# Optimization experiments

Hardware: AMD Instinct MI355X
Metric: run time of the kernel (lower is better)

The kernel has to match this reference:

```python
import jax, jax.numpy as jnp
import numpy as np

GROUP = 4      # number of groups in the batch dim
SHARED_GP = 4  # conv groups for q/k 1x1 convs
C = 512
N = 4096
B = 4          # B_all = GROUP * B = 16
EPS_LN = 1e-6
EPS_Z = 1e-6


def _phi(x):
    return jax.nn.relu(x) + 1.0


def _grouped_1x1(x, W):
    # x: [B, C, N], W: [g, C/g, C/g] block-diagonal 1x1 conv weights
    Bx, Cx, Nx = x.shape
    g = W.shape[0]
    xg = x.reshape(Bx, g, Cx // g, Nx)
    return jnp.einsum('goc,bgcn->bgon', W, xg).reshape(Bx, Cx, Nx)


def _ln(x, w, b, eps=EPS_LN):
    m = jnp.mean(x, axis=-1, keepdims=True)
    v = jnp.mean(jnp.square(x - m), axis=-1, keepdims=True)
    return (x - m) * jax.lax.rsqrt(v + eps) * w + b


def setup_inputs() -> dict:
    key = jax.random.key(0)
    ks = jax.random.split(key, 12)
    cg = C // SHARED_GP
    s = 1.0 / np.sqrt(C)
    return {
        'x': jax.random.normal(ks[0], (GROUP * B, C, N), dtype=jnp.float32),
        'Wq': jax.random.normal(ks[1], (SHARED_GP, cg, cg), dtype=jnp.float32) / np.sqrt(cg),
        'Wk': jax.random.normal(ks[2], (SHARED_GP, cg, cg), dtype=jnp.float32) / np.sqrt(cg),
        'Wv': jax.random.normal(ks[3], (C, C), dtype=jnp.float32) * s,
        'Wphi': jax.random.normal(ks[4], (C, C), dtype=jnp.float32) * s,
        'ln1_w': jnp.ones((C,), dtype=jnp.float32),
        'ln1_b': jnp.zeros((C,), dtype=jnp.float32),
        'fc1_w': jax.random.normal(ks[5], (4 * C, C), dtype=jnp.float32) * s,
        'fc1_b': jnp.zeros((4 * C,), dtype=jnp.float32),
        'fc2_w': jax.random.normal(ks[6], (C, 4 * C), dtype=jnp.float32) / np.sqrt(4 * C),
        'fc2_b': jnp.zeros((C,), dtype=jnp.float32),
        'ln2_w': jnp.ones((C,), dtype=jnp.float32),
        'ln2_b': jnp.zeros((C,), dtype=jnp.float32),
    }


def reference(x, Wq, Wk, Wv, Wphi, ln1_w, ln1_b, fc1_w, fc1_b, fc2_w, fc2_b, ln2_w, ln2_b):
    B_all, Cc, Nn = x.shape
    g = GROUP
    Bb = B_all // g
    first, rest = x[:Bb], x[Bb:]             # [B,C,N], [M,C,N] with M=(g-1)*B
    M = (g - 1) * Bb

    q = _phi(_grouped_1x1(rest, Wq))          # [M,C,N]
    k0 = _phi(_grouped_1x1(first, Wk))        # [B,C,N]
    v0 = jnp.einsum('oc,bcn->bon', Wv, first)  # [B,C,N]
    phi_first = jnp.einsum('oc,bcn->bon', Wphi, first)
    phi_rest = jnp.einsum('oc,bcn->bon', Wphi, rest)

    # expand first-group k/v across the (g-1) query groups
    k = jnp.broadcast_to(k0[None], (g - 1, Bb, Cc, Nn)).reshape(M, Cc, Nn)
    v = jnp.broadcast_to(v0[None], (g - 1, Bb, Cc, Nn)).reshape(M, Cc, Nn)

    Qg = jnp.broadcast_to(k0.mean(axis=2, keepdims=True)[None],
                          (g - 1, Bb, Cc, 1)).reshape(M, Cc, 1)
    alpha = jax.nn.softmax(jnp.sum(Qg * k, axis=1, keepdims=True), axis=-1) * Nn  # [M,1,N]
    k_hat = k * alpha

    # linear attention: kv = k_hat @ v^T / sqrt(C)
    kv = jnp.einsum('mcn,mdn->mcd', k_hat, v) / jnp.sqrt(jnp.asarray(Cc, x.dtype))  # [M,C,C]
    k_sum = jnp.sum(k_hat, axis=-1)                                  # [M,C]
    z = 1.0 / (jnp.einsum('mcn,mc->mn', q, k_sum)[:, None, :] + EPS_Z)  # [M,1,N]
    y = jnp.einsum('mcn,mcd->mdn', q, kv) * z * phi_rest              # [M,C,N]

    y_first = jnp.mean(y, axis=0, keepdims=True) * phi_first          # [B,C,N]
    out_first = _ln((first + y_first).transpose(0, 2, 1), ln1_w, ln1_b)  # [B,N,C]
    h = jax.nn.relu(out_first @ fc1_w.T + fc1_b)
    out_first = out_first + h @ fc2_w.T + fc2_b
    out_first = jax.nn.relu(_ln(out_first, ln2_w, ln2_b))
    out_first = out_first.transpose(0, 2, 1)                          # [B,C,N]
    return jnp.concatenate([out_first, rest], axis=0)
```

## Files before the change

kernel.cpp:

```cpp
#include <hip/hip_runtime.h>

#define N_DIM 4096
#define C_DIM 512
#define CN_ ((long)C_DIM * (long)N_DIM)

typedef unsigned short ushort_t;
typedef __attribute__((ext_vector_type(8))) short bf16x8;
typedef __attribute__((ext_vector_type(4))) float f32x4;

typedef const __attribute__((address_space(1))) unsigned int* gas_t;
typedef __attribute__((address_space(3))) unsigned int* las_t;
#define GLOAD(g, l) __builtin_amdgcn_global_load_lds((gas_t)(g), (las_t)(l), 16, 0, 0)

__device__ __forceinline__ ushort_t f2b(float f) {
    unsigned u = __builtin_bit_cast(unsigned, f);
    u += 0x7fffu + ((u >> 16) & 1u);
    return (ushort_t)(u >> 16);
}
__device__ __forceinline__ float b2f(ushort_t s) {
    return __builtin_bit_cast(float, (unsigned)s << 16);
}

enum { EPI_NONE = 0, EPI_PHI = 1, EPI_RELU_BIAS = 2, EPI_RES_BIAS = 3, EPI_PRE = 4 };

#define STAGE(q, koff) { \
    GLOAD(ap0 + (koff), &Als[q][la0]); \
    GLOAD(ap1 + (koff), &Als[q][la1]); \
    GLOAD(bp0 + (koff), &Bls[q][la0]); \
    GLOAD(bp1 + (koff), &Bls[q][la1]); }

#define COMPUTE(q) { \
    bf16x8 af[4], bfv[4]; \
    _Pragma("unroll") for (int m_ = 0; m_ < 4; ++m_) \
        af[m_] = *(const bf16x8*)&Als[q][(wr + m_ * 16 + fr) * 32 + rsw]; \
    _Pragma("unroll") for (int nf_ = 0; nf_ < 4; ++nf_) \
        bfv[nf_] = *(const bf16x8*)&Bls[q][(wc + nf_ * 16 + fr) * 32 + rsw]; \
    _Pragma("unroll") for (int m_ = 0; m_ < 4; ++m_) \
        _Pragma("unroll") for (int nf_ = 0; nf_ < 4; ++nf_) \
            acc[m_][nf_] = __builtin_amdgcn_mfma_f32_16x16x32_bf16( \
                af[m_], bfv[nf_], acc[m_][nf_], 0, 0, 0); }

#define KLOOP(K_) { \
    STAGE(0, 0); \
    __syncthreads(); \
    int kk_ = 0; \
    while (true) { \
        if (kk_ + 32 < (K_)) STAGE(1, kk_ + 32); \
        COMPUTE(0); \
        __syncthreads(); \
        kk_ += 32; \
        if (kk_ >= (K_)) break; \
        if (kk_ + 32 < (K_)) STAGE(0, kk_ + 32); \
        COMPUTE(1); \
        __syncthreads(); \
        kk_ += 32; \
        if (kk_ >= (K_)) break; \
    } }

template<int EPI, bool GROUPED, bool OBF, bool DEN>
__global__ __launch_bounds__(256, 3) void mfma_gemm(
    const ushort_t* __restrict__ Wb, const ushort_t* __restrict__ A,
    void* __restrict__ OUTV, const float* __restrict__ bias,
    const ushort_t* __restrict__ auxb, const float* __restrict__ auxf,
    int K, int O, int a_rstride, long a_zstride, long o_zstride, long auxb_zstride,
    int xt, int yt)
{
    __shared__ ushort_t Als[2][128 * 32];
    __shared__ ushort_t Bls[2][128 * 32];
    const int tid = threadIdx.x;

    const int L = blockIdx.x;
    const int gpx = (gridDim.x >> 3) / xt;
    const int xcd = L & 7;
    const int j = L >> 3;
    const int xtile = j % xt;
    const int g = xcd * gpx + j / xt;
    const int ytile = g % yt;
    const int z = g / yt;

    const int o0 = xtile * 128;
    const int n0 = ytile * 128;
    const ushort_t* Az = A + (long)z * a_zstride;
    const ushort_t* Wp = Wb;
    int kbase = 0, obase = o0;
    if (GROUPED) { int gg = o0 >> 7; Wp = Wb + (long)gg * (128 * 128); kbase = gg << 7; obase = 0; }

    const int w = tid >> 6, l = tid & 63;
    const int lr = l >> 2, lg = l & 3;
    const int rA0 = w * 32 + lr, rA1 = w * 32 + 16 + lr;
    const int gA0 = lg ^ ((rA0 >> 1) & 3), gA1 = lg ^ ((rA1 >> 1) & 3);
    const ushort_t* ap0 = Az + (long)(n0 + rA0) * a_rstride + kbase + gA0 * 8;
    const ushort_t* ap1 = Az + (long)(n0 + rA1) * a_rstride + kbase + gA1 * 8;
    const ushort_t* bp0 = Wp + (long)(obase + rA0) * K + gA0 * 8;
    const ushort_t* bp1 = Wp + (long)(obase + rA1) * K + gA1 * 8;
    const int la0 = (w * 32) * 32, la1 = (w * 32 + 16) * 32;

    const int wr = (w >> 1) * 64, wc = (w & 1) * 64;
    const int fr = l & 15, ks = l >> 4;
    const int rsw = (ks ^ ((fr >> 1) & 3)) << 3;

    f32x4 acc[4][4];
#pragma unroll
    for (int m = 0; m < 4; ++m)
#pragma unroll
        for (int nf = 0; nf < 4; ++nf) acc[m][nf] = f32x4{0.f, 0.f, 0.f, 0.f};

    KLOOP(K);

    float dsum[4][4];
    if (DEN) {
#pragma unroll
        for (int m = 0; m < 4; ++m)
#pragma unroll
            for (int j2 = 0; j2 < 4; ++j2) dsum[m][j2] = 0.f;
    }

#pragma unroll
    for (int m = 0; m < 4; ++m) {
#pragma unroll
        for (int nf = 0; nf < 4; ++nf) {
            const int oo = o0 + wc + nf * 16 + fr;
            float bval = 0.f;
            if (EPI == EPI_RELU_BIAS || EPI == EPI_RES_BIAS) bval = bias[oo];
            float kw = 0.f;
            if (DEN) kw = bias[((z & 3) << 9) + oo];
#pragma unroll
            for (int j2 = 0; j2 < 4; ++j2) {
                const int nn = n0 + wr + m * 16 + ks * 4 + j2;
                const long ridx = (long)nn * O + oo;
                float v = acc[m][nf][j2];
                if (EPI == EPI_PHI)            v = fmaxf(v, 0.f) + 1.f;
                else if (EPI == EPI_RELU_BIAS) v = fmaxf(v + bval, 0.f);
                else if (EPI == EPI_RES_BIAS)  v = v + bval + b2f(auxb[(long)z * auxb_zstride + ridx]);
                else if (EPI == EPI_PRE)       v = b2f(auxb[(long)z * auxb_zstride + ridx]) + auxf[ridx] * v;
                if (DEN) dsum[m][j2] += v * kw;
                if (OBF) ((ushort_t*)OUTV)[(long)z * o_zstride + ridx] = f2b(v);
                else     ((float*)OUTV)[(long)z * o_zstride + ridx] = v;
            }
        }
    }

    if (DEN) {
#pragma unroll
        for (int m = 0; m < 4; ++m)
#pragma unroll
            for (int j2 = 0; j2 < 4; ++j2) {
                float d = dsum[m][j2];
                d += __shfl_xor(d, 1); d += __shfl_xor(d, 2);
                d += __shfl_xor(d, 4); d += __shfl_xor(d, 8);
                if (fr == 0) {
                    const int nn = n0 + wr + m * 16 + ks * 4 + j2;
                    atomicAdd((float*)&auxf[(long)z * N_DIM + nn], d);
                }
            }
    }
}

__global__ __launch_bounds__(256, 3) void kv_mfma(
    const ushort_t* __restrict__ v0c, const ushort_t* __restrict__ khat,
    float* __restrict__ kvb)
{
    __shared__ ushort_t Als[2][128 * 32];
    __shared__ ushort_t Bls[2][128 * 32];
    const int tid = threadIdx.x;
    const int L = blockIdx.x;
    const int gpx = (gridDim.x >> 3) >> 2;
    const int xcd = L & 7;
    const int j = L >> 3;
    const int xtile = j & 3;
    const int g = xcd * gpx + (j >> 2);
    const int ytile = g & 3;
    const int z = g >> 2;
    const int c0 = xtile * 128, d0 = ytile * 128;
    const int b = z >> 3, nch = z & 7;

    const int w = tid >> 6, l = tid & 63;
    const int lr = l >> 2, lg = l & 3;
    const int rA0 = w * 32 + lr, rA1 = w * 32 + 16 + lr;
    const int gA0 = lg ^ ((rA0 >> 1) & 3), gA1 = lg ^ ((rA1 >> 1) & 3);
    const ushort_t* Ab = v0c + (long)b * CN_ + nch * 512;
    const ushort_t* Bb = khat + (long)b * CN_ + nch * 512;
    const ushort_t* ap0 = Ab + (long)(d0 + rA0) * N_DIM + gA0 * 8;
    const ushort_t* ap1 = Ab + (long)(d0 + rA1) * N_DIM + gA1 * 8;
    const ushort_t* bp0 = Bb + (long)(c0 + rA0) * N_DIM + gA0 * 8;
    const ushort_t* bp1 = Bb + (long)(c0 + rA1) * N_DIM + gA1 * 8;
    const int la0 = (w * 32) * 32, la1 = (w * 32 + 16) * 32;

    const int wr = (w >> 1) * 64, wc = (w & 1) * 64;
    const int fr = l & 15, ks = l >> 4;
    const int rsw = (ks ^ ((fr >> 1) & 3)) << 3;

    f32x4 acc[4][4];
#pragma unroll
    for (int m = 0; m < 4; ++m)
#pragma unroll
        for (int nf = 0; nf < 4; ++nf) acc[m][nf] = f32x4{0.f, 0.f, 0.f, 0.f};

    KLOOP(512);

    float* KV = kvb + (long)b * 262144;
#pragma unroll
    for (int m = 0; m < 4; ++m)
#pragma unroll
        for (int nf = 0; nf < 4; ++nf) {
            const int cc = c0 + wc + nf * 16 + fr;
#pragma unroll
            for (int j2 = 0; j2 < 4; ++j2) {
                const int dd = d0 + wr + m * 16 + ks * 4 + j2;
                atomicAdd(&KV[(long)dd * 512 + cc], acc[m][nf][j2]);
            }
        }
}

__global__ __launch_bounds__(256, 2) void ybar_gemm(
    const ushort_t* __restrict__ q12, const ushort_t* __restrict__ kvT,
    const ushort_t* __restrict__ xT12, const ushort_t* __restrict__ Wphi_b,
    const float* __restrict__ den12, ushort_t* __restrict__ y12)
{
    __shared__ ushort_t Als[2][128 * 32];
    __shared__ ushort_t Bls[2][128 * 32];
    const int tid = threadIdx.x;
    const int L = blockIdx.x;
    const int gpx = (gridDim.x >> 3) >> 2;
    const int xcd = L & 7;
    const int j = L >> 3;
    const int xtile = j & 3;
    const int g = xcd * gpx + (j >> 2);
    const int ytile = g & 31;
    const int mm = g >> 5;
    const int o0 = xtile * 128, n0 = ytile * 128;

    const int w = tid >> 6, l = tid & 63;
    const int lr = l >> 2, lg = l & 3;
    const int rA0 = w * 32 + lr, rA1 = w * 32 + 16 + lr;
    const int gA0 = lg ^ ((rA0 >> 1) & 3), gA1 = lg ^ ((rA1 >> 1) & 3);
    const long aoff0 = (long)(n0 + rA0) * 512 + gA0 * 8;
    const long aoff1 = (long)(n0 + rA1) * 512 + gA1 * 8;
    const long boff0 = (long)(o0 + rA0) * 512 + gA0 * 8;
    const long boff1 = (long)(o0 + rA1) * 512 + gA1 * 8;
    const int la0 = (w * 32) * 32, la1 = (w * 32 + 16) * 32;

    const int wr = (w >> 1) * 64, wc = (w & 1) * 64;
    const int fr = l & 15, ks = l >> 4;
    const int rsw = (ks ^ ((fr >> 1) & 3)) << 3;

    f32x4 acc[4][4];
#pragma unroll
    for (int m = 0; m < 4; ++m)
#pragma unroll
        for (int nf = 0; nf < 4; ++nf) acc[m][nf] = f32x4{0.f, 0.f, 0.f, 0.f};

    const ushort_t* ap0 = xT12 + (long)mm * CN_ + aoff0;
    const ushort_t* ap1 = xT12 + (long)mm * CN_ + aoff1;
    const ushort_t* bp0 = Wphi_b + boff0;
    const ushort_t* bp1 = Wphi_b + boff1;
    KLOOP(512);

    uint2 ph[4][4];
#pragma unroll
    for (int m = 0; m < 4; ++m)
#pragma unroll
        for (int nf = 0; nf < 4; ++nf) {
            ph[m][nf].x = (unsigned)f2b(acc[m][nf][0]) | ((unsigned)f2b(acc[m][nf][1]) << 16);
            ph[m][nf].y = (unsigned)f2b(acc[m][nf][2]) | ((unsigned)f2b(acc[m][nf][3]) << 16);
            acc[m][nf] = f32x4{0.f, 0.f, 0.f, 0.f};
        }

    ap0 = q12 + (long)mm * CN_ + aoff0;
    ap1 = q12 + (long)mm * CN_ + aoff1;
    bp0 = kvT + (long)(mm & 3) * 262144 + boff0;
    bp1 = kvT + (long)(mm & 3) * 262144 + boff1;
    KLOOP(512);

    const float* D = den12 + (long)mm * N_DIM;
    ushort_t* Y = y12 + (long)mm * CN_;
#pragma unroll
    for (int m = 0; m < 4; ++m) {
        float zr[4];
#pragma unroll
        for (int j2 = 0; j2 < 4; ++j2)
            zr[j2] = 1.f / (D[n0 + wr + m * 16 + ks * 4 + j2] + 1e-6f);
#pragma unroll
        for (int nf = 0; nf < 4; ++nf) {
            const int oo = o0 + wc + nf * 16 + fr;
            float pv[4];
            pv[0] = b2f((ushort_t)(ph[m][nf].x & 0xffff));
            pv[1] = b2f((ushort_t)(ph[m][nf].x >> 16));
            pv[2] = b2f((ushort_t)(ph[m][nf].y & 0xffff));
            pv[3] = b2f((ushort_t)(ph[m][nf].y >> 16));
#pragma unroll
            for (int j2 = 0; j2 < 4; ++j2) {
                const int nn = n0 + wr + m * 16 + ks * 4 + j2;
                Y[(long)nn * 512 + oo] = f2b(acc[m][nf][j2] * zr[j2] * pv[j2]);
            }
        }
    }
}

__global__ __launch_bounds__(256) void ybar_reduce(
    const ushort_t* __restrict__ y12, float* __restrict__ ybar)
{
    const long i = ((long)blockIdx.x * 256 + threadIdx.x) * 8;
    float s[8] = {0.f, 0.f, 0.f, 0.f, 0.f, 0.f, 0.f, 0.f};
    for (int mm = 0; mm < 12; ++mm) {
        uint4 u = *(const uint4*)&y12[(long)mm * CN_ + i];
        const ushort_t* us = (const ushort_t*)&u;
#pragma unroll
        for (int j = 0; j < 8; ++j) s[j] += b2f(us[j]);
    }
#pragma unroll
    for (int j = 0; j < 8; ++j) s[j] *= (1.f / 12.f);
    *(float4*)&ybar[i] = make_float4(s[0], s[1], s[2], s[3]);
    *(float4*)&ybar[i + 4] = make_float4(s[4], s[5], s[6], s[7]);
}

__global__ __launch_bounds__(256) void cvt_scale(
    const float* __restrict__ in, ushort_t* __restrict__ out)
{
    const float s = 0.044194173824159216f;
    int i = (blockIdx.x * 256 + threadIdx.x) * 4;
    float4 v = *(const float4*)&in[i];
    union { ushort_t sh[4]; uint2 u; } p;
    p.sh[0] = f2b(v.x * s); p.sh[1] = f2b(v.y * s);
    p.sh[2] = f2b(v.z * s); p.sh[3] = f2b(v.w * s);
    *(uint2*)&out[i] = p.u;
}

template<int ALPHA>
__global__ __launch_bounds__(256) void transpose_b2b(
    const ushort_t* __restrict__ in, ushort_t* __restrict__ out,
    const float* __restrict__ alpha)
{
    __shared__ ushort_t t[64][72];
    const int tid = threadIdx.x;
    const int n0 = blockIdx.x * 64, c0 = blockIdx.y * 64, z = blockIdx.z;
    const ushort_t* I = in + (long)z * CN_;
    ushort_t* O = out + (long)z * CN_;
    const int r = tid >> 2, s8 = (tid & 3) * 16;
    uint4 u0 = *(const uint4*)&I[(long)(n0 + r) * 512 + c0 + s8];
    uint4 u1 = *(const uint4*)&I[(long)(n0 + r) * 512 + c0 + s8 + 8];
    *(uint4*)&t[r][s8] = u0;
    *(uint4*)&t[r][s8 + 8] = u1;
    __syncthreads();
    union { ushort_t sh[16]; uint4 u[2]; } p;
#pragma unroll
    for (int i = 0; i < 16; ++i) {
        ushort_t v = t[s8 + i][r];
        if (ALPHA) v = f2b(b2f(v) * alpha[(long)z * N_DIM + n0 + s8 + i]);
        p.sh[i] = v;
    }
    uint4* dst = (uint4*)&O[(long)(c0 + r) * N_DIM + n0 + s8];
    dst[0] = p.u[0]; dst[1] = p.u[1];
}

__global__ __launch_bounds__(256) void cvt_all(
    const float* __restrict__ s0, ushort_t* __restrict__ d0,
    const float* __restrict__ s1, ushort_t* __restrict__ d1,
    const float* __restrict__ s2, ushort_t* __restrict__ d2,
    const float* __restrict__ s3, ushort_t* __restrict__ d3,
    const float* __restrict__ s4, ushort_t* __restrict__ d4,
    const float* __restrict__ s5, ushort_t* __restrict__ d5)
{
    long i = ((long)blockIdx.x * 256 + threadIdx.x) * 4;
    const float* s; ushort_t* d; long off;
    if (i < 65536)        { s = s0; d = d0; off = i; }
    else if (i < 131072)  { s = s1; d = d1; off = i - 65536; }
    else if (i < 393216)  { s = s2; d = d2; off = i - 131072; }
    else if (i < 655360)  { s = s3; d = d3; off = i - 393216; }
    else if (i < 1703936) { s = s4; d = d4; off = i - 655360; }
    else                  { s = s5; d = d5; off = i - 1703936; }
    float4 v = *(const float4*)&s[off];
    union { ushort_t sh[4]; uint2 u; } p;
    p.sh[0] = f2b(v.x); p.sh[1] = f2b(v.y); p.sh[2] = f2b(v.z); p.sh[3] = f2b(v.w);
    *(uint2*)&d[off] = p.u;
}

template<int PASSZ>
__global__ __launch_bounds__(256) void transpose_f2b(
    const float* __restrict__ in, ushort_t* __restrict__ out,
    int rows, int cols, long in_z, long out_z, float* __restrict__ passout)
{
    __shared__ float t[64][65];
    const int tid = threadIdx.x;
    const int n0 = blockIdx.x * 64, c0 = blockIdx.y * 64;
    const int z = blockIdx.z;
    const float* I = in + (long)z * in_z;
    ushort_t* Ot = out + (long)z * out_z;
    const int r = tid >> 2, s4 = (tid & 3) * 16;
    float4 raw[4];
#pragma unroll
    for (int i = 0; i < 16; i += 4) {
        float4 v = *(const float4*)&I[(long)(c0 + r) * cols + n0 + s4 + i];
        raw[i >> 2] = v;
        t[r][s4 + i] = v.x; t[r][s4 + i + 1] = v.y;
        t[r][s4 + i + 2] = v.z; t[r][s4 + i + 3] = v.w;
    }
    if (PASSZ && z >= 4) {
        float* P = passout + (long)z * in_z + (long)(c0 + r) * cols + n0 + s4;
#pragma unroll
        for (int i = 0; i < 4; ++i) *(float4*)&P[i * 4] = raw[i];
    }
    __syncthreads();
    union { ushort_t s[16]; uint4 u[2]; } pk;
#pragma unroll
    for (int i = 0; i < 16; ++i) pk.s[i] = f2b(t[s4 + i][r]);
    uint4* dst = (uint4*)&Ot[(long)(n0 + r) * rows + c0 + s4];
    dst[0] = pk.u[0]; dst[1] = pk.u[1];
}

__global__ __launch_bounds__(256) void colreduce_part(
    const ushort_t* __restrict__ X, const float* __restrict__ wgt,
    float* __restrict__ part)
{
    const int ns = blockIdx.x, b = blockIdx.y;
    const int tid = threadIdx.x;
    const int w = tid >> 6, l = tid & 63;
    const int c8 = l * 8;
    const ushort_t* Xb = X + (long)b * CN_;
    float acc[8] = {0.f, 0.f, 0.f, 0.f, 0.f, 0.f, 0.f, 0.f};
    for (int r = w; r < 128; r += 4) {
        const int n = ns * 128 + r;
        uint4 u = *(const uint4*)&Xb[(long)n * C_DIM + c8];
        const ushort_t* us = (const ushort_t*)&u;
        const float wv = wgt ? wgt[(long)b * N_DIM + n] : 1.f;
#pragma unroll
        for (int i = 0; i < 8; ++i) acc[i] += b2f(us[i]) * wv;
    }
    __shared__ float red[4][512];
#pragma unroll
    for (int i = 0; i < 8; ++i) red[w][c8 + i] = acc[i];
    __syncthreads();
    for (int c = tid; c < 512; c += 256) {
        part[((long)ns * 4 + b) * C_DIM + c] =
            red[0][c] + red[1][c] + red[2][c] + red[3][c];
    }
}

__global__ __launch_bounds__(256) void colreduce_fin(
    const float* __restrict__ part, float* __restrict__ out, float scale)
{
    int b = blockIdx.x;
    for (int c = threadIdx.x; c < 512; c += 256) {
        float s = 0.f;
        for (int ns = 0; ns < 32; ++ns) s += part[((long)ns * 4 + b) * C_DIM + c];
        out[b * C_DIM + c] = s * scale;
    }
}

__global__ __launch_bounds__(256) void dot_rows(
    const ushort_t* __restrict__ X, const float* __restrict__ w,
    float* __restrict__ out)
{
    const int tid = threadIdx.x;
    const int rn = tid >> 2, cs = (tid & 3) * 128;
    const int z = blockIdx.y;
    const int n = blockIdx.x * 64 + rn;
    const ushort_t* row = X + (long)z * CN_ + (long)n * C_DIM;
    const float* wz = w + (long)(z & 3) * C_DIM;
    float s = 0.f;
    for (int i = 0; i < 128; i += 8) {
        uint4 u = *(const uint4*)&row[cs + i];
        const ushort_t* us = (const ushort_t*)&u;
#pragma unroll
        for (int k2 = 0; k2 < 8; ++k2) s += b2f(us[k2]) * wz[cs + i + k2];
    }
    s += __shfl_xor(s, 1); s += __shfl_xor(s, 2);
    if ((tid & 3) == 0) out[(long)z * N_DIM + n] = s;
}

__global__ __launch_bounds__(256) void softmax_alpha(
    const float* __restrict__ logits, float* __restrict__ alpha)
{
    int b = blockIdx.x, tid = threadIdx.x;
    const float* L = logits + (long)b * N_DIM;
    float* A = alpha + (long)b * N_DIM;
    float lv[16];
    float mx = -3.4e38f;
#pragma unroll
    for (int i = 0; i < 4; i++) {
        float4 v = *(const float4*)&L[tid * 4 + i * 1024];
        lv[4 * i + 0] = v.x; lv[4 * i + 1] = v.y; lv[4 * i + 2] = v.z; lv[4 * i + 3] = v.w;
        mx = fmaxf(mx, fmaxf(fmaxf(v.x, v.y), fmaxf(v.z, v.w)));
    }
    __shared__ float red[8];
    float m = mx;
#pragma unroll
    for (int off = 32; off; off >>= 1) m = fmaxf(m, __shfl_down(m, off, 64));
    int wid = tid >> 6, lane = tid & 63;
    if (lane == 0) red[wid] = m;
    __syncthreads();
    m = fmaxf(fmaxf(red[0], red[1]), fmaxf(red[2], red[3]));
    float e[16], s = 0.f;
#pragma unroll
    for (int i = 0; i < 16; i++) { e[i] = expf(lv[i] - m); s += e[i]; }
#pragma unroll
    for (int off = 32; off; off >>= 1) s += __shfl_down(s, off, 64);
    if (lane == 0) red[4 + wid] = s;
    __syncthreads();
    float S = red[4] + red[5] + red[6] + red[7];
    float sc = 4096.f / S;
#pragma unroll
    for (int i = 0; i < 4; i++)
        *(float4*)&A[tid * 4 + i * 1024] =
            make_float4(e[4 * i] * sc, e[4 * i + 1] * sc, e[4 * i + 2] * sc, e[4 * i + 3] * sc);
}

template<int RELU, int OBF, int IBF>
__global__ __launch_bounds__(256) void ln_row(
    const void* __restrict__ inv, const float* __restrict__ g,
    const float* __restrict__ bt, void* __restrict__ outv)
{
    const int tid = threadIdx.x;
    const int r = tid >> 3, cs = (tid & 7) * 64;
    const long base = (((long)blockIdx.y * N_DIM) + blockIdx.x * 32 + r) * C_DIM + cs;
    float vv[64];
    float s = 0.f, s2 = 0.f;
    if (IBF) {
        const ushort_t* I = (const ushort_t*)inv + base;
#pragma unroll
        for (int i = 0; i < 8; ++i) {
            uint4 u = *(const uint4*)&I[i * 8];
            const ushort_t* us = (const ushort_t*)&u;
#pragma unroll
            for (int jj = 0; jj < 8; ++jj) {
                float f = b2f(us[jj]); vv[i * 8 + jj] = f; s += f; s2 += f * f;
            }
        }
    } else {
        const float* I = (const float*)inv + base;
#pragma unroll
        for (int i = 0; i < 16; ++i) {
            float4 v = *(const float4*)&I[i * 4];
            vv[i * 4] = v.x; vv[i * 4 + 1] = v.y; vv[i * 4 + 2] = v.z; vv[i * 4 + 3] = v.w;
            s += v.x + v.y + v.z + v.w;
            s2 += v.x * v.x + v.y * v.y + v.z * v.z + v.w * v.w;
        }
    }
#pragma unroll
    for (int off = 1; off < 8; off <<= 1) { s += __shfl_xor(s, off); s2 += __shfl_xor(s2, off); }
    const float mean = s * (1.f / 512.f);
    const float var = s2 * (1.f / 512.f) - mean * mean;
    const float rs = rsqrtf(var + 1e-6f);
#pragma unroll
    for (int i = 0; i < 64; i += 4) {
        float o[4];
#pragma unroll
        for (int jj = 0; jj < 4; ++jj) {
            float ov = (vv[i + jj] - mean) * rs * g[cs + i + jj] + bt[cs + i + jj];
            if (RELU) ov = fmaxf(ov, 0.f);
            o[jj] = ov;
        }
        if (OBF) {
            union { ushort_t s4[4]; uint2 u; } p;
            p.s4[0] = f2b(o[0]); p.s4[1] = f2b(o[1]); p.s4[2] = f2b(o[2]); p.s4[3] = f2b(o[3]);
            *(uint2*)&((ushort_t*)outv)[base + i] = p.u;
        } else {
            *(float4*)&((float*)outv)[base + i] = make_float4(o[0], o[1], o[2], o[3]);
        }
    }
}

__global__ __launch_bounds__(256) void ln_tr(
    const ushort_t* __restrict__ in, const float* __restrict__ g,
    const float* __restrict__ bt, float* __restrict__ out)
{
    __shared__ float t[32][513];
    const int tid = threadIdx.x;
    const int r = tid >> 3;
    const int lc = (tid & 7) * 8;
    const int z = blockIdx.y;
    const long n = (long)blockIdx.x * 32 + r;
    const ushort_t* I = in + ((long)z * N_DIM + n) * C_DIM;
    float vv[64];
    float s = 0.f, s2 = 0.f;
#pragma unroll
    for (int i = 0; i < 8; ++i) {
        const int c = i * 64 + lc;
        uint4 u = *(const uint4*)&I[c];
        const ushort_t* us = (const ushort_t*)&u;
#pragma unroll
        for (int jj = 0; jj < 8; ++jj) {
            float f = b2f(us[jj]); vv[i * 8 + jj] = f; s += f; s2 += f * f;
        }
    }
#pragma unroll
    for (int off = 1; off < 8; off <<= 1) { s += __shfl_xor(s, off); s2 += __shfl_xor(s2, off); }
    const float mean = s * (1.f / 512.f);
    const float var = s2 * (1.f / 512.f) - mean * mean;
    const float rs = rsqrtf(var + 1e-6f);
#pragma unroll
    for (int i = 0; i < 8; ++i) {
        const int c = i * 64 + lc;
#pragma unroll
        for (int jj = 0; jj < 8; ++jj) {
            float o = (vv[i * 8 + jj] - mean) * rs * g[c + jj] + bt[c + jj];
            t[r][c + jj] = fmaxf(o, 0.f);
        }
    }
    __syncthreads();
    float* O = out + (long)z * CN_ + (long)blockIdx.x * 32;
    for (int c = tid; c < 512; c += 256) {
        float* dst = O + (long)c * N_DIM;
#pragma unroll
        for (int i = 0; i < 32; i += 4)
            *(float4*)&dst[i] = make_float4(t[i][c], t[i + 1][c], t[i + 2][c], t[i + 3][c]);
    }
}

extern "C" void kernel_launch(void* const* d_in, const int* in_sizes, int n_in,
                              void* d_out, int out_size, void* d_ws, size_t ws_size,
                              hipStream_t stream)
{
    const float* x     = (const float*)d_in[0];
    const float* Wq    = (const float*)d_in[1];
    const float* Wk    = (const float*)d_in[2];
    const float* Wv    = (const float*)d_in[3];
    const float* Wphi  = (const float*)d_in[4];
    const float* ln1_w = (const float*)d_in[5];
    const float* ln1_b = (const float*)d_in[6];
    const float* fc1_w = (const float*)d_in[7];
    const float* fc1_bias = (const float*)d_in[8];
    const float* fc2_w = (const float*)d_in[9];
    const float* fc2_bias = (const float*)d_in[10];
    const float* ln2_w = (const float*)d_in[11];
    const float* ln2_b = (const float*)d_in[12];
    float* out = (float*)d_out;

    float* ws = (float*)d_ws;
    const long CN = CN_;
    ushort_t* xTfirst = (ushort_t*)ws;
    ushort_t* tln     = (ushort_t*)ws;
    ushort_t* xT12 = (ushort_t*)(ws + 2 * CN);
    ushort_t* hbuf4 = (ushort_t*)(ws + 2 * CN);
    ushort_t* q12   = (ushort_t*)(ws + 8 * CN);
    ushort_t* y12   = (ushort_t*)(ws + 14 * CN);
    ushort_t* k0b = (ushort_t*)(ws + 20 * CN);
    ushort_t* v0b = (ushort_t*)(ws + 22 * CN);
    ushort_t* pre_b = (ushort_t*)(ws + 20 * CN);
    ushort_t* khat = (ushort_t*)(ws + 24 * CN);
    ushort_t* v0c  = (ushort_t*)(ws + 26 * CN);
    ushort_t* ubuf_b = (ushort_t*)(ws + 24 * CN);
    float* ybar = ws + 32 * CN;
    float* kvb  = ws + 33 * CN;
    ushort_t* kvT = (ushort_t*)(ws + 33 * CN + 1048576);
    float* wb = ws + 33 * CN + 1572864;
    ushort_t* Wk_b   = (ushort_t*)(wb);
    ushort_t* Wq_b   = (ushort_t*)(wb + 32768);
    ushort_t* Wv_b   = (ushort_t*)(wb + 65536);
    ushort_t* Wphi_b = (ushort_t*)(wb + 196608);
    ushort_t* fc1_b16 = (ushort_t*)(wb + 327680);
    ushort_t* fc2_b16 = (ushort_t*)(wb + 851968);
    float* part   = wb + 1376256;
    float* Qg     = wb + 1441792;
    float* ksum   = wb + 1443840;
    float* logits = wb + 1445888;
    float* alpha  = wb + 1462272;
    float* den12  = wb + 1478656;

    dim3 blk(256);

    cvt_all<<<2688, blk, 0, stream>>>(Wk, Wk_b, Wq, Wq_b, Wv, Wv_b,
                                      Wphi, Wphi_b, fc1_w, fc1_b16, fc2_w, fc2_b16);
    hipMemsetAsync(kvb, 0, 1048576 * sizeof(float), stream);
    hipMemsetAsync(den12, 0, 49152 * sizeof(float), stream);

    transpose_f2b<1><<<dim3(64, 8, 16), blk, 0, stream>>>(
        x, xTfirst, 512, 4096, CN, CN, out);

    mfma_gemm<EPI_PHI, true, true, false><<<512, blk, 0, stream>>>(
        Wk_b, xTfirst, k0b, nullptr, nullptr, nullptr, 128, 512, 512, CN, CN, 0, 4, 32);
    mfma_gemm<EPI_NONE, false, true, false><<<512, blk, 0, stream>>>(
        Wv_b, xTfirst, v0b, nullptr, nullptr, nullptr, 512, 512, 512, CN, CN, 0, 4, 32);
    colreduce_part<<<dim3(32, 4), blk, 0, stream>>>(k0b, nullptr, part);
    colreduce_fin<<<4, blk, 0, stream>>>(part, Qg, 1.f / 4096.f);
    dot_rows<<<dim3(64, 4), blk, 0, stream>>>(k0b, Qg, logits);
    softmax_alpha<<<4, blk, 0, stream>>>(logits, alpha);
    colreduce_part<<<dim3(32, 4), blk, 0, stream>>>(k0b, alpha, part);
    colreduce_fin<<<4, blk, 0, stream>>>(part, ksum, 1.f);
    transpose_b2b<1><<<dim3(64, 8, 4), blk, 0, stream>>>(k0b, khat, alpha);
    transpose_b2b<0><<<dim3(64, 8, 4), blk, 0, stream>>>(v0b, v0c, nullptr);
    kv_mfma<<<512, blk, 0, stream>>>(v0c, khat, kvb);
    cvt_scale<<<1024, blk, 0, stream>>>(kvb, kvT);

    mfma_gemm<EPI_PHI, true, true, true><<<1536, blk, 0, stream>>>(
        Wq_b, xT12, q12, ksum, nullptr, den12, 128, 512, 512, CN, CN, 0, 4, 32);
    ybar_gemm<<<1536, blk, 0, stream>>>(q12, kvT, xT12, Wphi_b, den12, y12);
    ybar_reduce<<<1024, blk, 0, stream>>>(y12, ybar);

    mfma_gemm<EPI_PRE, false, true, false><<<512, blk, 0, stream>>>(
        Wphi_b, xTfirst, pre_b, nullptr, xTfirst, ybar, 512, 512, 512, CN, CN, CN, 4, 32);
    ln_row<0, 1, 1><<<dim3(128, 4), blk, 0, stream>>>(pre_b, ln1_w, ln1_b, tln);
    mfma_gemm<EPI_RELU_BIAS, false, true, false><<<2048, blk, 0, stream>>>(
        fc1_b16, tln, hbuf4, fc1_bias, nullptr, nullptr,
        512, 2048, 512, CN, 8388608, 0, 16, 32);
    mfma_gemm<EPI_RES_BIAS, false, true, false><<<512, blk, 0, stream>>>(
        fc2_b16, hbuf4, ubuf_b, fc2_bias, tln, nullptr,
        2048, 512, 2048, 8388608, CN, CN, 4, 32);
    ln_tr<<<dim3(128, 4), blk, 0, stream>>>(ubuf_b, ln2_w, ln2_b, out);
}
```

Measured before the change: 497.0 us.

## Fuse column reductions into epilogues and replace kv atomics with partial buffers

```diff
diff --git a/kernel.cpp b/kernel.cpp
--- a/kernel.cpp
+++ b/kernel.cpp
@@ -57,7 +57,7 @@
         if (kk_ >= (K_)) break; \
     } }
 
-template<int EPI, bool GROUPED, bool OBF, bool DEN>
+template<int EPI, bool GROUPED, bool OBF, bool DEN, bool QGS>
 __global__ __launch_bounds__(256, 3) void mfma_gemm(
     const ushort_t* __restrict__ Wb, const ushort_t* __restrict__ A,
     void* __restrict__ OUTV, const float* __restrict__ bias,
@@ -114,6 +114,11 @@
 #pragma unroll
             for (int j2 = 0; j2 < 4; ++j2) dsum[m][j2] = 0.f;
     }
+    float qsum[4];
+    if (QGS) {
+#pragma unroll
+        for (int nf = 0; nf < 4; ++nf) qsum[nf] = 0.f;
+    }
 
 #pragma unroll
     for (int m = 0; m < 4; ++m) {
@@ -134,6 +139,7 @@
                 else if (EPI == EPI_RES_BIAS)  v = v + bval + b2f(auxb[(long)z * auxb_zstride + ridx]);
                 else if (EPI == EPI_PRE)       v = b2f(auxb[(long)z * auxb_zstride + ridx]) + auxf[ridx] * v;
                 if (DEN) dsum[m][j2] += v * kw;
+                if (QGS) qsum[nf] += v;
                 if (OBF) ((ushort_t*)OUTV)[(long)z * o_zstride + ridx] = f2b(v);
                 else     ((float*)OUTV)[(long)z * o_zstride + ridx] = v;
             }
@@ -154,11 +160,23 @@
                 }
             }
     }
+    if (QGS) {
+#pragma unroll
+        for (int nf = 0; nf < 4; ++nf) {
+            float d = qsum[nf];
+            d += __shfl_xor(d, 16);
+            d += __shfl_xor(d, 32);
+            if (ks == 0) {
+                const int oo = o0 + wc + nf * 16 + fr;
+                atomicAdd((float*)&auxf[((long)z << 9) + oo], d);
+            }
+        }
+    }
 }
 
 __global__ __launch_bounds__(256, 3) void kv_mfma(
     const ushort_t* __restrict__ v0c, const ushort_t* __restrict__ khat,
-    float* __restrict__ kvb)
+    float* __restrict__ kvp)
 {
     __shared__ ushort_t Als[2][128 * 32];
     __shared__ ushort_t Bls[2][128 * 32];
@@ -198,7 +216,7 @@
 
     KLOOP(512);
 
-    float* KV = kvb + (long)b * 262144;
+    float* KV = kvp + ((long)(nch * 4 + b)) * 262144;
 #pragma unroll
     for (int m = 0; m < 4; ++m)
 #pragma unroll
@@ -207,9 +225,28 @@
 #pragma unroll
             for (int j2 = 0; j2 < 4; ++j2) {
                 const int dd = d0 + wr + m * 16 + ks * 4 + j2;
-                atomicAdd(&KV[(long)dd * 512 + cc], acc[m][nf][j2]);
+                KV[(long)dd * 512 + cc] = acc[m][nf][j2];
             }
         }
+}
+
+__global__ __launch_bounds__(256) void cvt_scale8(
+    const float* __restrict__ kvp, ushort_t* __restrict__ out)
+{
+    const float s = 0.044194173824159216f;
+    const long i = ((long)blockIdx.x * 256 + threadIdx.x) * 4;
+    const int b = (int)(i >> 18);
+    const long j = i & 262143;
+    float4 a = make_float4(0.f, 0.f, 0.f, 0.f);
+#pragma unroll
+    for (int nch = 0; nch < 8; ++nch) {
+        float4 v = *(const float4*)&kvp[((long)(nch * 4 + b)) * 262144 + j];
+        a.x += v.x; a.y += v.y; a.z += v.z; a.w += v.w;
+    }
+    union { ushort_t sh[4]; uint2 u; } p;
+    p.sh[0] = f2b(a.x * s); p.sh[1] = f2b(a.y * s);
+    p.sh[2] = f2b(a.z * s); p.sh[3] = f2b(a.w * s);
+    *(uint2*)&out[i] = p.u;
 }
 
 __global__ __launch_bounds__(256, 2) void ybar_gemm(
@@ -314,22 +351,10 @@
     *(float4*)&ybar[i + 4] = make_float4(s[4], s[5], s[6], s[7]);
 }
 
-__global__ __launch_bounds__(256) void cvt_scale(
-    const float* __restrict__ in, ushort_t* __restrict__ out)
-{
-    const float s = 0.044194173824159216f;
-    int i = (blockIdx.x * 256 + threadIdx.x) * 4;
-    float4 v = *(const float4*)&in[i];
-    union { ushort_t sh[4]; uint2 u; } p;
-    p.sh[0] = f2b(v.x * s); p.sh[1] = f2b(v.y * s);
-    p.sh[2] = f2b(v.z * s); p.sh[3] = f2b(v.w * s);
-    *(uint2*)&out[i] = p.u;
-}
-
 template<int ALPHA>
 __global__ __launch_bounds__(256) void transpose_b2b(
     const ushort_t* __restrict__ in, ushort_t* __restrict__ out,
-    const float* __restrict__ alpha)
+    const float* __restrict__ alpha, float* __restrict__ ksum)
 {
     __shared__ ushort_t t[64][72];
     const int tid = threadIdx.x;
@@ -351,6 +376,16 @@
     }
     uint4* dst = (uint4*)&O[(long)(c0 + r) * N_DIM + n0 + s8];
     dst[0] = p.u[0]; dst[1] = p.u[1];
+    if (ALPHA) {
+        const int c = tid & 63, q = tid >> 6;
+        float s = 0.f;
+#pragma unroll
+        for (int i = 0; i < 16; ++i) {
+            const int n = q * 16 + i;
+            s += b2f(t[n][c]) * alpha[(long)z * N_DIM + n0 + n];
+        }
+        atomicAdd(&ksum[((long)z << 9) + c0 + c], s);
+    }
 }
 
 __global__ __launch_bounds__(256) void cvt_all(
@@ -408,48 +443,9 @@
     dst[0] = pk.u[0]; dst[1] = pk.u[1];
 }
 
-__global__ __launch_bounds__(256) void colreduce_part(
-    const ushort_t* __restrict__ X, const float* __restrict__ wgt,
-    float* __restrict__ part)
-{
-    const int ns = blockIdx.x, b = blockIdx.y;
-    const int tid = threadIdx.x;
-    const int w = tid >> 6, l = tid & 63;
-    const int c8 = l * 8;
-    const ushort_t* Xb = X + (long)b * CN_;
-    float acc[8] = {0.f, 0.f, 0.f, 0.f, 0.f, 0.f, 0.f, 0.f};
-    for (int r = w; r < 128; r += 4) {
-        const int n = ns * 128 + r;
-        uint4 u = *(const uint4*)&Xb[(long)n * C_DIM + c8];
-        const ushort_t* us = (const ushort_t*)&u;
-        const float wv = wgt ? wgt[(long)b * N_DIM + n] : 1.f;
-#pragma unroll
-        for (int i = 0; i < 8; ++i) acc[i] += b2f(us[i]) * wv;
-    }
-    __shared__ float red[4][512];
-#pragma unroll
-    for (int i = 0; i < 8; ++i) red[w][c8 + i] = acc[i];
-    __syncthreads();
-    for (int c = tid; c < 512; c += 256) {
-        part[((long)ns * 4 + b) * C_DIM + c] =
-            red[0][c] + red[1][c] + red[2][c] + red[3][c];
-    }
-}
-
-__global__ __launch_bounds__(256) void colreduce_fin(
-    const float* __restrict__ part, float* __restrict__ out, float scale)
-{
-    int b = blockIdx.x;
-    for (int c = threadIdx.x; c < 512; c += 256) {
-        float s = 0.f;
-        for (int ns = 0; ns < 32; ++ns) s += part[((long)ns * 4 + b) * C_DIM + c];
-        out[b * C_DIM + c] = s * scale;
-    }
-}
-
 __global__ __launch_bounds__(256) void dot_rows(
     const ushort_t* __restrict__ X, const float* __restrict__ w,
-    float* __restrict__ out)
+    float* __restrict__ out, float scale)
 {
     const int tid = threadIdx.x;
     const int rn = tid >> 2, cs = (tid & 3) * 128;
@@ -465,7 +461,7 @@
         for (int k2 = 0; k2 < 8; ++k2) s += b2f(us[k2]) * wz[cs + i + k2];
     }
     s += __shfl_xor(s, 1); s += __shfl_xor(s, 2);
-    if ((tid & 3) == 0) out[(long)z * N_DIM + n] = s;
+    if ((tid & 3) == 0) out[(long)z * N_DIM + n] = s * scale;
 }
 
 __global__ __launch_bounds__(256) void softmax_alpha(
@@ -641,59 +637,54 @@
     ushort_t* v0c  = (ushort_t*)(ws + 26 * CN);
     ushort_t* ubuf_b = (ushort_t*)(ws + 24 * CN);
     float* ybar = ws + 32 * CN;
-    float* kvb  = ws + 33 * CN;
-    ushort_t* kvT = (ushort_t*)(ws + 33 * CN + 1048576);
-    float* wb = ws + 33 * CN + 1572864;
+    float* kvp  = ws + 33 * CN;
+    ushort_t* kvT = (ushort_t*)(ws + 33 * CN + 8388608);
+    float* wb = ws + 33 * CN + 8388608 + 524288;
     ushort_t* Wk_b   = (ushort_t*)(wb);
     ushort_t* Wq_b   = (ushort_t*)(wb + 32768);
     ushort_t* Wv_b   = (ushort_t*)(wb + 65536);
     ushort_t* Wphi_b = (ushort_t*)(wb + 196608);
     ushort_t* fc1_b16 = (ushort_t*)(wb + 327680);
     ushort_t* fc2_b16 = (ushort_t*)(wb + 851968);
-    float* part   = wb + 1376256;
-    float* Qg     = wb + 1441792;
-    float* ksum   = wb + 1443840;
-    float* logits = wb + 1445888;
-    float* alpha  = wb + 1462272;
-    float* den12  = wb + 1478656;
+    float* Qg     = wb + 1376256;
+    float* ksum   = wb + 1378304;
+    float* logits = wb + 1380352;
+    float* alpha  = wb + 1396736;
+    float* den12  = wb + 1413120;
 
     dim3 blk(256);
 
     cvt_all<<<2688, blk, 0, stream>>>(Wk, Wk_b, Wq, Wq_b, Wv, Wv_b,
                                       Wphi, Wphi_b, fc1_w, fc1_b16, fc2_w, fc2_b16);
-    hipMemsetAsync(kvb, 0, 1048576 * sizeof(float), stream);
+    hipMemsetAsync(Qg, 0, 4096 * sizeof(float), stream);
     hipMemsetAsync(den12, 0, 49152 * sizeof(float), stream);
 
     transpose_f2b<1><<<dim3(64, 8, 16), blk, 0, stream>>>(
         x, xTfirst, 512, 4096, CN, CN, out);
 
-    mfma_gemm<EPI_PHI, true, true, false><<<512, blk, 0, stream>>>(
-        Wk_b, xTfirst, k0b, nullptr, nullptr, nullptr, 128, 512, 512, CN, CN, 0, 4, 32);
-    mfma_gemm<EPI_NONE, false, true, false><<<512, blk, 0, stream>>>(
+    mfma_gemm<EPI_PHI, true, true, false, true><<<512, blk, 0, stream>>>(
+        Wk_b, xTfirst, k0b, nullptr, nullptr, Qg, 128, 512, 512, CN, CN, 0, 4, 32);
+    mfma_gemm<EPI_NONE, false, true, false, false><<<512, blk, 0, stream>>>(
         Wv_b, xTfirst, v0b, nullptr, nullptr, nullptr, 512, 512, 512, CN, CN, 0, 4, 32);
-    colreduce_part<<<dim3(32, 4), blk, 0, stream>>>(k0b, nullptr, part);
-    colreduce_fin<<<4, blk, 0, stream>>>(part, Qg, 1.f / 4096.f);
-    dot_rows<<<dim3(64, 4), blk, 0, stream>>>(k0b, Qg, logits);
+    dot_rows<<<dim3(64, 4), blk, 0, stream>>>(k0b, Qg, logits, 1.f / 4096.f);
     softmax_alpha<<<4, blk, 0, stream>>>(logits, alpha);
-    colreduce_part<<<dim3(32, 4), blk, 0, stream>>>(k0b, alpha, part);
-    colreduce_fin<<<4, blk, 0, stream>>>(part, ksum, 1.f);
-    transpose_b2b<1><<<dim3(64, 8, 4), blk, 0, stream>>>(k0b, khat, alpha);
-    transpose_b2b<0><<<dim3(64, 8, 4), blk, 0, stream>>>(v0b, v0c, nullptr);
-    kv_mfma<<<512, blk, 0, stream>>>(v0c, khat, kvb);
-    cvt_scale<<<1024, blk, 0, stream>>>(kvb, kvT);
-
-    mfma_gemm<EPI_PHI, true, true, true><<<1536, blk, 0, stream>>>(
+    transpose_b2b<1><<<dim3(64, 8, 4), blk, 0, stream>>>(k0b, khat, alpha, ksum);
+    transpose_b2b<0><<<dim3(64, 8, 4), blk, 0, stream>>>(v0b, v0c, nullptr, nullptr);
+    kv_mfma<<<512, blk, 0, stream>>>(v0c, khat, kvp);
+    cvt_scale8<<<1024, blk, 0, stream>>>(kvp, kvT);
+
+    mfma_gemm<EPI_PHI, true, true, true, false><<<1536, blk, 0, stream>>>(
         Wq_b, xT12, q12, ksum, nullptr, den12, 128, 512, 512, CN, CN, 0, 4, 32);
     ybar_gemm<<<1536, blk, 0, stream>>>(q12, kvT, xT12, Wphi_b, den12, y12);
     ybar_reduce<<<1024, blk, 0, stream>>>(y12, ybar);
 
-    mfma_gemm<EPI_PRE, false, true, false><<<512, blk, 0, stream>>>(
+    mfma_gemm<EPI_PRE, false, true, false, false><<<512, blk, 0, stream>>>(
         Wphi_b, xTfirst, pre_b, nullptr, xTfirst, ybar, 512, 512, 512, CN, CN, CN, 4, 32);
     ln_row<0, 1, 1><<<dim3(128, 4), blk, 0, stream>>>(pre_b, ln1_w, ln1_b, tln);
-    mfma_gemm<EPI_RELU_BIAS, false, true, false><<<2048, blk, 0, stream>>>(
+    mfma_gemm<EPI_RELU_BIAS, false, true, false, false><<<2048, blk, 0, stream>>>(
         fc1_b16, tln, hbuf4, fc1_bias, nullptr, nullptr,
         512, 2048, 512, CN, 8388608, 0, 16, 32);
-    mfma_gemm<EPI_RES_BIAS, false, true, false><<<512, blk, 0, stream>>>(
+    mfma_gemm<EPI_RES_BIAS, false, true, false, false><<<512, blk, 0, stream>>>(
         fc2_b16, hbuf4, ubuf_b, fc2_bias, tln, nullptr,
         2048, 512, 2048, 8388608, CN, CN, 4, 32);
     ln_tr<<<dim3(128, 4), blk, 0, stream>>>(ubuf_b, ln2_w, ln2_b, out);
```

After: 468.7 us. -5.7%, faster.
